# Kernel optimization log

Hardware: AMD Instinct MI355X
Metric: run time of the kernel (lower is better)

## Reference

```python
import jax, jax.numpy as jnp
import numpy as np

H = 64
N_G, E_G = 30000, 60000
N_LG, E_LG = 60000, 60000


def setup_inputs() -> dict:
    key = jax.random.key(0)
    ks = jax.random.split(key, 30)
    rn = lambda k, s, sc=0.05: jax.random.normal(k, s, jnp.float32) * sc
    return {
        "gx": jax.random.normal(ks[0], (N_G, 20), jnp.float32),
        "g_edge_index": jax.random.randint(ks[1], (2, E_G), 0, N_G, jnp.int32),
        "g_edge_attr": jax.random.uniform(ks[2], (E_G, 4), dtype=jnp.float32),
        "lgx": jax.random.normal(ks[3], (N_LG, 5), jnp.float32),
        "lg_edge_index": jax.random.randint(ks[4], (2, E_LG), 0, N_LG, jnp.int32),
        "lg_edge_attr": jax.random.uniform(ks[5], (E_LG, 1), dtype=jnp.float32),
        "adduct": jax.random.normal(ks[6], (3,), jnp.float32),
        "lin0_w": rn(ks[7], (20, H)), "lin0_b": rn(ks[8], (H,)),
        "g_nn_w1": rn(ks[9], (4, H)), "g_nn_b1": rn(ks[10], (H,)),
        "g_nn_w2": rn(ks[11], (H, H * H), 0.01), "g_nn_b2": rn(ks[12], (H * H,), 0.01),
        "g_root": rn(ks[13], (H, H)), "g_bias": rn(ks[14], (H,)),
        "lin0_lg_w": rn(ks[15], (5, H)), "lin0_lg_b": rn(ks[16], (H,)),
        "lg_nn_w1": rn(ks[17], (1, H)), "lg_nn_b1": rn(ks[18], (H,)),
        "lg_nn_w2": rn(ks[19], (H, H * H), 0.01), "lg_nn_b2": rn(ks[20], (H * H,), 0.01),
        "lg_root": rn(ks[21], (H, H)), "lg_bias": rn(ks[22], (H,)),
        "bott_w": rn(ks[23], (H + H + 3, 384)), "bott_b": rn(ks[24], (384,)),
        "lin1_w": rn(ks[25], (384, 384)), "lin1_b": rn(ks[26], (384,)),
        "lin2_w": rn(ks[27], (384, 1)), "lin2_b": rn(ks[28], (1,)),
    }


def _ecc_branch(x_in, edge_index, edge_attr, w1, b1, w2, b2, root, bias, n_iters, num_nodes):
    """N iterations of NNConv(aggr='mean') + ReLU, then sum pool over nodes."""
    src, tgt = edge_index[0], edge_index[1]  # source->target flow (PyG default)
    # edge MLP -> per-edge [in, out] weight (edge_attr is loop-invariant, compute once)
    W = (jax.nn.relu(edge_attr @ w1 + b1) @ w2 + b2).reshape(-1, H, H)  # [E, H, H]
    cnt = jnp.maximum(
        jax.ops.segment_sum(jnp.ones((tgt.shape[0],), x_in.dtype), tgt, num_segments=num_nodes),
        1.0,
    )
    x = x_in
    for _ in range(n_iters):
        msg = jnp.einsum('ei,eio->eo', x[src], W)  # gather + batched matvec
        agg = jax.ops.segment_sum(msg, tgt, num_segments=num_nodes) / cnt[:, None]  # scatter-mean
        x = jax.nn.relu(x @ root + agg + bias)  # root transform + bias (NNConv defaults)
    return x.sum(axis=0)  # sum pooling -> [H]


def reference(gx, g_edge_index, g_edge_attr, lgx, lg_edge_index, lg_edge_attr, adduct,
              lin0_w, lin0_b, g_nn_w1, g_nn_b1, g_nn_w2, g_nn_b2, g_root, g_bias,
              lin0_lg_w, lin0_lg_b, lg_nn_w1, lg_nn_b1, lg_nn_w2, lg_nn_b2, lg_root, lg_bias,
              bott_w, bott_b, lin1_w, lin1_b, lin2_w, lin2_b):
    out_g = _ecc_branch(jax.nn.relu(gx @ lin0_w + lin0_b), g_edge_index, g_edge_attr,
                        g_nn_w1, g_nn_b1, g_nn_w2, g_nn_b2, g_root, g_bias, 3, N_G)
    out_lg = _ecc_branch(jax.nn.relu(lgx @ lin0_lg_w + lin0_lg_b), lg_edge_index, lg_edge_attr,
                         lg_nn_w1, lg_nn_b1, lg_nn_w2, lg_nn_b2, lg_root, lg_bias, 3, N_LG)
    out = jnp.concatenate([out_g, out_lg, adduct], axis=-1)  # [131]
    out = jax.nn.relu(out @ bott_w + bott_b)
    for _ in range(6):
        out = jax.nn.relu(out @ lin1_w + lin1_b)
    return out @ lin2_w + lin2_b  # [1]
```

## Files before the change

kernel.cpp:

```cpp
#include <hip/hip_runtime.h>

typedef unsigned short u16;
using short8_t  = __attribute__((ext_vector_type(8)))  short;
using float16_t = __attribute__((ext_vector_type(16))) float;
using float2v   = __attribute__((ext_vector_type(2)))  float;

#define NKT 260
#define DEG_CAP 32

__device__ __forceinline__ float bf2f(u16 b) { return __uint_as_float(((unsigned)b) << 16); }
__device__ __forceinline__ u16 f2bf(float f) {
  unsigned u = __float_as_uint(f);
  return (u16)((u + 0x7fffu + ((u >> 16) & 1u)) >> 16);
}

union U8 { short8_t s; uint4 v; unsigned u[4]; };

__device__ __forceinline__ short8_t scale8r(U8 xr, float2v h2) {
  U8 out;
  #pragma unroll
  for (int p = 0; p < 4; ++p) {
    float2v r;
    r[0] = __uint_as_float(xr.u[p] << 16);
    r[1] = __uint_as_float(xr.u[p] & 0xffff0000u);
    r = r * h2;
    out.u[p] = __builtin_amdgcn_perm(__float_as_uint(r[1]), __float_as_uint(r[0]), 0x07060302);
  }
  return out.s;
}

template<int IN>
__device__ __forceinline__ void affine_body(
    const float* __restrict__ Xin, const float* __restrict__ W, const float* __restrict__ Bv,
    u16* __restrict__ Xout, int N, int gid)
{
  int n = gid >> 6, o = gid & 63;
  if (n >= N) return;
  float acc = Bv[o];
  #pragma unroll
  for (int i = 0; i < IN; ++i)
    acc = fmaf(Xin[n * IN + i], W[i * 64 + o], acc);
  Xout[gid] = f2bf(fmaxf(acc, 0.f));
}

__global__ __launch_bounds__(256) void affine_all_kernel(
    const float* __restrict__ gx, const float* __restrict__ l0w, const float* __restrict__ l0b, u16* __restrict__ xg,
    const float* __restrict__ lgx, const float* __restrict__ llw, const float* __restrict__ llb, u16* __restrict__ xl,
    const float* __restrict__ gea, const float* __restrict__ gw1, const float* __restrict__ gb1, u16* __restrict__ hg,
    const float* __restrict__ lea, const float* __restrict__ lw1, const float* __restrict__ lb1, u16* __restrict__ hl,
    int B0, int B1, int B2, int NG, int NLG, int EG, int ELG)
{
  int b = blockIdx.x, t = threadIdx.x;
  if (b < B0)       affine_body<20>(gx, l0w, l0b, xg, NG, b * 256 + t);
  else if (b < B1)  affine_body<5>(lgx, llw, llb, xl, NLG, (b - B0) * 256 + t);
  else if (b < B2)  affine_body<4>(gea, gw1, gb1, hg, EG, (b - B1) * 256 + t);
  else              affine_body<1>(lea, lw1, lb1, hl, ELG, (b - B2) * 256 + t);
}

__device__ __forceinline__ void bpack_body(
    const float* __restrict__ w2, const float* __restrict__ b2, u16* __restrict__ Bp, int gid)
{
  if (gid >= NKT * 128) return;
  int lane = gid & 63;
  int nt = (gid >> 6) & 1;
  int kt = gid >> 7;
  int o = nt * 32 + (lane & 31);
  int kbase = kt * 16 + (lane >> 5) * 8;
  u16 vals[8];
  #pragma unroll
  for (int j = 0; j < 8; ++j) {
    int k = kbase + j;
    vals[j] = f2bf((k < 4096) ? w2[(k >> 6) * 4096 + (k & 63) * 64 + o]
                              : b2[(k - 4096) * 64 + o]);
  }
  uint4 pack;
  pack.x = (unsigned)vals[0] | ((unsigned)vals[1] << 16);
  pack.y = (unsigned)vals[2] | ((unsigned)vals[3] << 16);
  pack.z = (unsigned)vals[4] | ((unsigned)vals[5] << 16);
  pack.w = (unsigned)vals[6] | ((unsigned)vals[7] << 16);
  *(uint4*)(Bp + (size_t)gid * 8) = pack;
}

__device__ __forceinline__ void rootpack_body(const float* __restrict__ root, u16* __restrict__ Rp, int gid)
{
  if (gid >= 512) return;
  int lane = gid & 63;
  int nt = (gid >> 6) & 1;
  int kt = gid >> 7;
  int o = nt * 32 + (lane & 31);
  int kbase = kt * 16 + (lane >> 5) * 8;
  u16 vals[8];
  #pragma unroll
  for (int j = 0; j < 8; ++j) vals[j] = f2bf(root[(kbase + j) * 64 + o]);
  uint4 pack;
  pack.x = (unsigned)vals[0] | ((unsigned)vals[1] << 16);
  pack.y = (unsigned)vals[2] | ((unsigned)vals[3] << 16);
  pack.z = (unsigned)vals[4] | ((unsigned)vals[5] << 16);
  pack.w = (unsigned)vals[6] | ((unsigned)vals[7] << 16);
  *(uint4*)(Rp + (size_t)gid * 8) = pack;
}

__global__ __launch_bounds__(256) void pack_all_kernel(
    const float* __restrict__ gw2, const float* __restrict__ gb2, u16* __restrict__ bpg,
    const float* __restrict__ lw2, const float* __restrict__ lb2, u16* __restrict__ bpl,
    const float* __restrict__ groot, u16* __restrict__ rpg,
    const float* __restrict__ lroot, u16* __restrict__ rpl)
{
  int b = blockIdx.x, t = threadIdx.x;
  if (b < 130)       bpack_body(gw2, gb2, bpg, b * 256 + t);
  else if (b < 260)  bpack_body(lw2, lb2, bpl, (b - 130) * 256 + t);
  else if (b < 262)  rootpack_body(groot, rpg, (b - 260) * 256 + t);
  else               rootpack_body(lroot, rpl, (b - 262) * 256 + t);
}

__device__ __forceinline__ void hist_body(
    const int* __restrict__ eidx, int* __restrict__ cnt, int* __restrict__ elist, int E, int e)
{
  if (e < E) {
    int tg = eidx[E + e];
    int pos = atomicAdd(cnt + tg, 1);
    if (pos < DEG_CAP) elist[(size_t)tg * DEG_CAP + pos] = e;
  }
}

__global__ __launch_bounds__(256) void hist_kernel(
    const int* __restrict__ eig, int* __restrict__ cg, int* __restrict__ elg, int Eg, int nbg,
    const int* __restrict__ eil, int* __restrict__ cl, int* __restrict__ ell, int El)
{
  int b = blockIdx.x, t = threadIdx.x;
  if (b < nbg) hist_body(eig, cg, elg, Eg, b * 256 + t);
  else         hist_body(eil, cl, ell, El, (b - nbg) * 256 + t);
}

__global__ __launch_bounds__(256, 2) void msg_gemm_kernel(
    const u16* __restrict__ Xg, const u16* __restrict__ Hg, const u16* __restrict__ Bg,
    const int* __restrict__ eig, u16* __restrict__ Mg, int Eg, int nbg,
    const u16* __restrict__ Xl, const u16* __restrict__ Hl, const u16* __restrict__ Bl,
    const int* __restrict__ eil, u16* __restrict__ Ml, int El)
{
  __shared__ __align__(16) u16 sB[4][8192];

  const int b = blockIdx.x;
  const u16 *X, *Hh, *Bp; const int* eidx; u16* msg; int E, e0;
  if (b < nbg) { X = Xg; Hh = Hg; Bp = Bg; eidx = eig; msg = Mg; E = Eg; e0 = b * 256; }
  else         { X = Xl; Hh = Hl; Bp = Bl; eidx = eil; msg = Ml; E = El; e0 = (b - nbg) * 256; }

  const int t = threadIdx.x;
  const int lane = t & 63;
  const int wid = t >> 6;
  const int ml = lane & 31;
  const int q  = lane >> 5;

  #pragma unroll
  for (int c0 = 0; c0 < 3; ++c0) {
    const u16* src = Bp + (size_t)c0 * 8192 + (size_t)wid * 2048 + (size_t)lane * 8;
    u16* dst = &sB[c0][wid * 2048];
    #pragma unroll
    for (int d = 0; d < 4; ++d)
      __builtin_amdgcn_global_load_lds((const __attribute__((address_space(1))) void*)(src + d * 512),
                                       (__attribute__((address_space(3))) void*)(dst + d * 512), 16, 0, 0);
  }

  const int ea  = e0 + wid * 64 + ml;
  const int eb  = ea + 32;
  const int eac = ea < E ? ea : E - 1;
  const int ebc = eb < E ? eb : E - 1;
  const int sa  = eidx[eac], sb = eidx[ebc];

  U8 xra[4], xrb[4];
  {
    const u16* xpa = X + (size_t)sa * 64 + q * 8;
    const u16* xpb = X + (size_t)sb * 64 + q * 8;
    #pragma unroll
    for (int s = 0; s < 4; ++s) {
      xra[s].v = *(const uint4*)(xpa + s * 16);
      xrb[s].v = *(const uint4*)(xpb + s * 16);
    }
  }

  const uint4* ha4 = (const uint4*)(Hh + (size_t)eac * 64);
  const uint4* hb4 = (const uint4*)(Hh + (size_t)ebc * 64);
  uint4 hc0 = ha4[0], hn0 = ha4[1];
  uint4 hc1 = hb4[0], hn1 = hb4[1];

  float16_t acc00, acc01, acc10, acc11;
  #pragma unroll
  for (int i = 0; i < 16; ++i) { acc00[i] = 0.f; acc01[i] = 0.f; acc10[i] = 0.f; acc11[i] = 0.f; }

  const u16* bsrc = Bp + (size_t)3 * 8192 + (size_t)wid * 2048 + (size_t)lane * 8;

  const short8_t* sb8 = (const short8_t*)&sB[0][0];

  asm volatile("s_waitcnt vmcnt(0)" ::: "memory");
  __builtin_amdgcn_sched_barrier(0);
  __builtin_amdgcn_s_barrier();

  for (int g = 0; g < 8; ++g) {
    #pragma unroll
    for (int cc = 0; cc < 4; ++cc) {
      {
        #pragma unroll
        for (int d = 0; d < 4; ++d)
          __builtin_amdgcn_global_load_lds((const __attribute__((address_space(1))) void*)(bsrc + d * 512),
                                           (__attribute__((address_space(3))) void*)(&sB[(cc + 3) & 3][wid * 2048] + d * 512), 16, 0, 0);
        bsrc += 8192;
      }
      unsigned w0 = ((const unsigned*)&hc0)[cc];
      unsigned w1 = ((const unsigned*)&hc1)[cc];
      const int sbase = (cc & 3) * 1024;
      #pragma unroll
      for (int hh = 0; hh < 2; ++hh) {
        float2v h20, h21;
        h20[0] = h20[1] = bf2f((u16)(hh ? (w0 >> 16) : (w0 & 0xffffu)));
        h21[0] = h21[1] = bf2f((u16)(hh ? (w1 >> 16) : (w1 & 0xffffu)));
        #pragma unroll
        for (int tt = 0; tt < 4; ++tt) {
          short8_t b0 = sb8[sbase + (hh * 4 + tt) * 128 + lane];
          short8_t b1 = sb8[sbase + (hh * 4 + tt) * 128 + 64 + lane];
          short8_t a0 = scale8r(xra[tt], h20);
          short8_t a1 = scale8r(xrb[tt], h21);
          acc00 = __builtin_amdgcn_mfma_f32_32x32x16_bf16(a0, b0, acc00, 0, 0, 0);
          acc01 = __builtin_amdgcn_mfma_f32_32x32x16_bf16(a0, b1, acc01, 0, 0, 0);
          acc10 = __builtin_amdgcn_mfma_f32_32x32x16_bf16(a1, b0, acc10, 0, 0, 0);
          acc11 = __builtin_amdgcn_mfma_f32_32x32x16_bf16(a1, b1, acc11, 0, 0, 0);
        }
      }
      asm volatile("s_waitcnt lgkmcnt(0)" ::: "memory");
      asm volatile("s_waitcnt vmcnt(8)" ::: "memory");
      __builtin_amdgcn_sched_barrier(0);
      __builtin_amdgcn_s_barrier();
    }
    hc0 = hn0; hc1 = hn1;
    if (g < 6) { hn0 = ha4[g + 2]; hn1 = hb4[g + 2]; }
  }

  {
    float2v h2; h2[0] = 1.0f; h2[1] = 1.0f;
    #pragma unroll
    for (int tt = 0; tt < 4; ++tt) {
      short8_t b0 = sb8[tt * 128 + lane];
      short8_t b1 = sb8[tt * 128 + 64 + lane];
      short8_t a0 = scale8r(xra[tt], h2);
      short8_t a1 = scale8r(xrb[tt], h2);
      acc00 = __builtin_amdgcn_mfma_f32_32x32x16_bf16(a0, b0, acc00, 0, 0, 0);
      acc01 = __builtin_amdgcn_mfma_f32_32x32x16_bf16(a0, b1, acc01, 0, 0, 0);
      acc10 = __builtin_amdgcn_mfma_f32_32x32x16_bf16(a1, b0, acc10, 0, 0, 0);
      acc11 = __builtin_amdgcn_mfma_f32_32x32x16_bf16(a1, b1, acc11, 0, 0, 0);
    }
  }

  #pragma unroll
  for (int reg = 0; reg < 16; ++reg) {
    int row = (reg & 3) + 8 * (reg >> 2) + 4 * q;
    int e1 = e0 + wid * 64 + row;
    int e2 = e1 + 32;
    if (e1 < E) {
      msg[(size_t)e1 * 64 + ml]      = f2bf(acc00[reg]);
      msg[(size_t)e1 * 64 + 32 + ml] = f2bf(acc01[reg]);
    }
    if (e2 < E) {
      msg[(size_t)e2 * 64 + ml]      = f2bf(acc10[reg]);
      msg[(size_t)e2 * 64 + 32 + ml] = f2bf(acc11[reg]);
    }
  }
}

__global__ __launch_bounds__(256, 4) void update_kernel(
    const u16* __restrict__ Xig, const u16* __restrict__ Mgg, const int* __restrict__ cg,
    const int* __restrict__ elg, const u16* __restrict__ rpg, const float* __restrict__ bg,
    u16* __restrict__ Xog, int Ng, int nbg,
    const u16* __restrict__ Xil, const u16* __restrict__ Mgl, const int* __restrict__ cl,
    const int* __restrict__ ell, const u16* __restrict__ rpl, const float* __restrict__ bl,
    u16* __restrict__ Xol, int Nl)
{
  const int b = blockIdx.x;
  const u16 *Xin, *rootp, *msg; const float *bias; const int *cnt, *elist;
  u16* Xout; int N, n0;
  if (b < nbg) { Xin=Xig; msg=Mgg; cnt=cg; elist=elg; rootp=rpg; bias=bg; Xout=Xog; N=Ng; n0=b*128; }
  else         { Xin=Xil; msg=Mgl; cnt=cl; elist=ell; rootp=rpl; bias=bl; Xout=Xol; N=Nl; n0=(b-nbg)*128; }

  const int t = threadIdx.x;
  const int lane = t & 63;
  const int wid = t >> 6;
  const int ml = lane & 31;
  const int q  = lane >> 5;
  const int nbase = n0 + wid * 32;

  const int na = nbase + ml;
  const int nac = na < N ? na : N - 1;

  U8 xr[4];
  {
    const u16* xp = Xin + (size_t)nac * 64 + q * 8;
    #pragma unroll
    for (int s = 0; s < 4; ++s) xr[s].v = *(const uint4*)(xp + s * 16);
  }
  U8 rp[8];
  {
    const uint4* rpv = (const uint4*)rootp;
    #pragma unroll
    for (int i = 0; i < 8; ++i) rp[i].v = rpv[i * 64 + lane];
  }
  const float bias0 = bias[ml], bias1 = bias[32 + ml];

  float16_t acc0, acc1;
  #pragma unroll
  for (int i = 0; i < 16; ++i) { acc0[i] = 0.f; acc1[i] = 0.f; }
  #pragma unroll
  for (int kt = 0; kt < 4; ++kt) {
    acc0 = __builtin_amdgcn_mfma_f32_32x32x16_bf16(xr[kt].s, rp[kt * 2 + 0].s, acc0, 0, 0, 0);
    acc1 = __builtin_amdgcn_mfma_f32_32x32x16_bf16(xr[kt].s, rp[kt * 2 + 1].s, acc1, 0, 0, 0);
  }

  #pragma unroll
  for (int reg = 0; reg < 16; ++reg) {
    int row = (reg & 3) + 8 * (reg >> 2) + 4 * q;
    int nn = nbase + row;
    if (nn < N) {
      int c = cnt[nn];
      int cc = c < DEG_CAP ? c : DEG_CAP;
      const int* ep = elist + (size_t)nn * DEG_CAP;
      float a0 = 0.f, a1 = 0.f;
      int j = 0;
      for (; j + 4 <= cc; j += 4) {
        int e0i = ep[j], e1i = ep[j + 1], e2i = ep[j + 2], e3i = ep[j + 3];
        u16 m00 = msg[(size_t)e0i * 64 + ml], m01 = msg[(size_t)e0i * 64 + 32 + ml];
        u16 m10 = msg[(size_t)e1i * 64 + ml], m11 = msg[(size_t)e1i * 64 + 32 + ml];
        u16 m20 = msg[(size_t)e2i * 64 + ml], m21 = msg[(size_t)e2i * 64 + 32 + ml];
        u16 m30 = msg[(size_t)e3i * 64 + ml], m31 = msg[(size_t)e3i * 64 + 32 + ml];
        a0 += bf2f(m00) + bf2f(m10) + bf2f(m20) + bf2f(m30);
        a1 += bf2f(m01) + bf2f(m11) + bf2f(m21) + bf2f(m31);
      }
      for (; j < cc; ++j) {
        int e = ep[j];
        a0 += bf2f(msg[(size_t)e * 64 + ml]);
        a1 += bf2f(msg[(size_t)e * 64 + 32 + ml]);
      }
      float rc = (c > 1) ? (1.0f / (float)c) : 1.0f;
      float o0 = fmaxf(acc0[reg] + a0 * rc + bias0, 0.f);
      float o1 = fmaxf(acc1[reg] + a1 * rc + bias1, 0.f);
      Xout[(size_t)nn * 64 + ml]      = f2bf(o0);
      Xout[(size_t)nn * 64 + 32 + ml] = f2bf(o1);
    }
  }
}

__device__ __forceinline__ void pool_body(const u16* __restrict__ X, float* __restrict__ out64,
                                          int nchunks, int bid, int t)
{
  __shared__ float red[64];
  if (t < 64) red[t] = 0.f;
  __syncthreads();
  int gid = bid * 256 + t;
  float s[8];
  #pragma unroll
  for (int j = 0; j < 8; ++j) s[j] = 0.f;
  for (int i = gid; i < nchunks; i += 256 * 256) {
    uint4 v = ((const uint4*)X)[i];
    s[0] += bf2f((u16)(v.x & 0xffffu)); s[1] += bf2f((u16)(v.x >> 16));
    s[2] += bf2f((u16)(v.y & 0xffffu)); s[3] += bf2f((u16)(v.y >> 16));
    s[4] += bf2f((u16)(v.z & 0xffffu)); s[5] += bf2f((u16)(v.z >> 16));
    s[6] += bf2f((u16)(v.w & 0xffffu)); s[7] += bf2f((u16)(v.w >> 16));
  }
  int cg = (gid & 7) * 8;
  #pragma unroll
  for (int j = 0; j < 8; ++j) atomicAdd(red + cg + j, s[j]);
  __syncthreads();
  if (t < 64) atomicAdd(out64 + t, red[t]);
}

__global__ __launch_bounds__(256) void pool_kernel(
    const u16* __restrict__ Xg, float* __restrict__ og, int ncg,
    const u16* __restrict__ Xl, float* __restrict__ ol, int ncl)
{
  int b = blockIdx.x, t = threadIdx.x;
  if (b < 256) pool_body(Xg, og, ncg, b, t);
  else         pool_body(Xl, ol, ncl, b - 256, t);
}

__global__ __launch_bounds__(256) void prep_head_kernel(
    const float* __restrict__ pg, const float* __restrict__ plg, const float* __restrict__ adduct,
    float* __restrict__ v)
{
  int t = threadIdx.x;
  if (t < 131) v[t] = (t < 64) ? pg[t] : (t < 128 ? plg[t - 64] : adduct[t - 128]);
}

__global__ __launch_bounds__(256) void gemv_relu_kernel(
    const float* __restrict__ in, const float* __restrict__ W, const float* __restrict__ b,
    float* __restrict__ out, int Ni, int No)
{
  __shared__ float red[16][17];
  int t = threadIdx.x;
  int ol = t & 15, ig = t >> 4;
  int o = blockIdx.x * 16 + ol;
  float s = 0.f;
  for (int i = ig; i < Ni; i += 16)
    s = fmaf(in[i], W[i * No + o], s);
  red[ig][ol] = s;
  __syncthreads();
  if (t < 16) {
    int oo = blockIdx.x * 16 + t;
    float acc = b[oo];
    #pragma unroll
    for (int g = 0; g < 16; ++g) acc += red[g][t];
    out[oo] = fmaxf(acc, 0.f);
  }
}

__global__ __launch_bounds__(384) void final_kernel(
    const float* __restrict__ u, const float* __restrict__ l2w, const float* __restrict__ l2b,
    float* __restrict__ out)
{
  __shared__ float wred[6];
  int t = threadIdx.x;
  float p = u[t] * l2w[t];
  #pragma unroll
  for (int off = 32; off > 0; off >>= 1) p += __shfl_down(p, off);
  if ((t & 63) == 0) wred[t >> 6] = p;
  __syncthreads();
  if (t == 0) {
    float s = l2b[0];
    #pragma unroll
    for (int i = 0; i < 6; ++i) s += wred[i];
    out[0] = s;
  }
}

extern "C" void kernel_launch(void* const* d_in, const int* in_sizes, int n_in,
                              void* d_out, int out_size, void* d_ws, size_t ws_size,
                              hipStream_t stream)
{
  const int NG = 30000, EG = 60000, NLG = 60000, ELG = 60000;

  const float* gx      = (const float*)d_in[0];
  const int*   g_ei    = (const int*)  d_in[1];
  const float* g_ea    = (const float*)d_in[2];
  const float* lgx     = (const float*)d_in[3];
  const int*   lg_ei   = (const int*)  d_in[4];
  const float* lg_ea   = (const float*)d_in[5];
  const float* adduct  = (const float*)d_in[6];
  const float* lin0_w  = (const float*)d_in[7];
  const float* lin0_b  = (const float*)d_in[8];
  const float* g_w1    = (const float*)d_in[9];
  const float* g_b1    = (const float*)d_in[10];
  const float* g_w2    = (const float*)d_in[11];
  const float* g_b2    = (const float*)d_in[12];
  const float* g_root  = (const float*)d_in[13];
  const float* g_bias  = (const float*)d_in[14];
  const float* l0lg_w  = (const float*)d_in[15];
  const float* l0lg_b  = (const float*)d_in[16];
  const float* lg_w1   = (const float*)d_in[17];
  const float* lg_b1   = (const float*)d_in[18];
  const float* lg_w2   = (const float*)d_in[19];
  const float* lg_b2   = (const float*)d_in[20];
  const float* lg_root = (const float*)d_in[21];
  const float* lg_bias = (const float*)d_in[22];
  const float* bott_w  = (const float*)d_in[23];
  const float* bott_b  = (const float*)d_in[24];
  const float* lin1_w  = (const float*)d_in[25];
  const float* lin1_b  = (const float*)d_in[26];
  const float* lin2_w  = (const float*)d_in[27];
  const float* lin2_b  = (const float*)d_in[28];

  char* p = (char*)d_ws;
  auto alloc = [&](size_t bytes) { char* r = p; p += (bytes + 255) & ~(size_t)255; return r; };
  u16*   xg_a   = (u16*)  alloc((size_t)NG  * 64 * 2);
  u16*   xg_b   = (u16*)  alloc((size_t)NG  * 64 * 2);
  u16*   xl_a   = (u16*)  alloc((size_t)NLG * 64 * 2);
  u16*   xl_b   = (u16*)  alloc((size_t)NLG * 64 * 2);
  u16*   h_g    = (u16*)  alloc((size_t)EG  * 64 * 2);
  u16*   h_l    = (u16*)  alloc((size_t)ELG * 64 * 2);
  u16*   bp_g   = (u16*)  alloc((size_t)NKT * 128 * 8 * 2 + 49152);
  u16*   bp_l   = (u16*)  alloc((size_t)NKT * 128 * 8 * 2 + 49152);
  u16*   rp_g   = (u16*)  alloc(512 * 8 * 2);
  u16*   rp_l   = (u16*)  alloc(512 * 8 * 2);
  u16*   msg_g  = (u16*)  alloc((size_t)EG  * 64 * 2);
  u16*   msg_l  = (u16*)  alloc((size_t)ELG * 64 * 2);
  int*   cnt_g  = (int*)  alloc((size_t)NG  * 4);
  int*   cnt_l  = (int*)  alloc((size_t)NLG * 4);
  int*   el_g   = (int*)  alloc((size_t)NG  * DEG_CAP * 4);
  int*   el_l   = (int*)  alloc((size_t)NLG * DEG_CAP * 4);
  float* pool_g = (float*)alloc(64 * 4);
  float* pool_l = (float*)alloc(64 * 4);
  float* hv     = (float*)alloc(131 * 4);
  float* h0     = (float*)alloc(384 * 4);
  float* h1     = (float*)alloc(384 * 4);

  const int B0 = NG * 64 / 256, B1 = B0 + NLG * 64 / 256, B2 = B1 + EG * 64 / 256;
  const int Btot = B2 + ELG * 64 / 256;
  affine_all_kernel<<<Btot, 256, 0, stream>>>(
      gx, lin0_w, lin0_b, xg_a, lgx, l0lg_w, l0lg_b, xl_a,
      g_ea, g_w1, g_b1, h_g, lg_ea, lg_w1, lg_b1, h_l,
      B0, B1, B2, NG, NLG, EG, ELG);
  pack_all_kernel<<<264, 256, 0, stream>>>(g_w2, g_b2, bp_g, lg_w2, lg_b2, bp_l,
                                           g_root, rp_g, lg_root, rp_l);
  hipMemsetAsync(cnt_g, 0, (size_t)((char*)cnt_l - (char*)cnt_g) + (size_t)NLG * 4, stream);
  const int nhg = (EG + 255) / 256, nhl = (ELG + 255) / 256;
  hist_kernel<<<nhg + nhl, 256, 0, stream>>>(g_ei, cnt_g, el_g, EG, nhg, lg_ei, cnt_l, el_l, ELG);

  const int nbg_m = (EG + 255) / 256, nbl_m = (ELG + 255) / 256;
  const int nbg_u = (NG + 127) / 128, nbl_u = (NLG + 127) / 128;
  u16 *xgc = xg_a, *xgn = xg_b, *xlc = xl_a, *xln = xl_b;
  for (int it = 0; it < 3; ++it) {
    msg_gemm_kernel<<<nbg_m + nbl_m, 256, 0, stream>>>(
        xgc, h_g, bp_g, g_ei, msg_g, EG, nbg_m,
        xlc, h_l, bp_l, lg_ei, msg_l, ELG);
    update_kernel<<<nbg_u + nbl_u, 256, 0, stream>>>(
        xgc, msg_g, cnt_g, el_g, rp_g, g_bias, xgn, NG, nbg_u,
        xlc, msg_l, cnt_l, el_l, rp_l, lg_bias, xln, NLG);
    u16* tmp = xgc; xgc = xgn; xgn = tmp;
    tmp = xlc; xlc = xln; xln = tmp;
  }

  hipMemsetAsync(pool_g, 0, (size_t)((char*)pool_l - (char*)pool_g) + 64 * 4, stream);
  pool_kernel<<<512, 256, 0, stream>>>(xgc, pool_g, NG * 8, xlc, pool_l, NLG * 8);

  prep_head_kernel<<<1, 256, 0, stream>>>(pool_g, pool_l, adduct, hv);
  gemv_relu_kernel<<<24, 256, 0, stream>>>(hv, bott_w, bott_b, h0, 131, 384);
  float* ua = h0; float* ub = h1;
  for (int L = 0; L < 6; ++L) {
    gemv_relu_kernel<<<24, 256, 0, stream>>>(ua, lin1_w, lin1_b, ub, 384, 384);
    float* tmp = ua; ua = ub; ub = tmp;
  }
  final_kernel<<<1, 384, 0, stream>>>(ua, lin2_w, lin2_b, (float*)d_out);
}
```

Baseline: 491.8 us.

## Fuse MLP head into single block kernel and fold memsets into kernels

Replaces the prep, seven gemv launches and final kernel with one 384-thread head kernel that reduces the per-block pool partials, then runs the bottleneck, six hidden layers and output layer, keeping activations in shared memory. Pool blocks now write partial sums instead of using global atomics, so the pool memset goes away. The count-buffer memset is folded into the affine kernel as extra zeroing blocks. This removes roughly ten launches and their gaps, but the head GEMVs now run on a single block that reads about 590KB of weights serially per layer.

```diff
diff --git a/kernel.cpp b/kernel.cpp
--- a/kernel.cpp
+++ b/kernel.cpp
@@ -48,13 +48,18 @@
     const float* __restrict__ lgx, const float* __restrict__ llw, const float* __restrict__ llb, u16* __restrict__ xl,
     const float* __restrict__ gea, const float* __restrict__ gw1, const float* __restrict__ gb1, u16* __restrict__ hg,
     const float* __restrict__ lea, const float* __restrict__ lw1, const float* __restrict__ lb1, u16* __restrict__ hl,
-    int B0, int B1, int B2, int NG, int NLG, int EG, int ELG)
+    int B0, int B1, int B2, int B3, int NG, int NLG, int EG, int ELG,
+    int* __restrict__ zero_ptr, int NZ)
 {
   int b = blockIdx.x, t = threadIdx.x;
   if (b < B0)       affine_body<20>(gx, l0w, l0b, xg, NG, b * 256 + t);
   else if (b < B1)  affine_body<5>(lgx, llw, llb, xl, NLG, (b - B0) * 256 + t);
   else if (b < B2)  affine_body<4>(gea, gw1, gb1, hg, EG, (b - B1) * 256 + t);
-  else              affine_body<1>(lea, lw1, lb1, hl, ELG, (b - B2) * 256 + t);
+  else if (b < B3)  affine_body<1>(lea, lw1, lb1, hl, ELG, (b - B2) * 256 + t);
+  else {
+    int idx = (b - B3) * 256 + t;
+    if (idx < NZ) zero_ptr[idx] = 0;
+  }
 }
 
 __device__ __forceinline__ void bpack_body(
@@ -345,7 +350,7 @@
   }
 }
 
-__device__ __forceinline__ void pool_body(const u16* __restrict__ X, float* __restrict__ out64,
+__device__ __forceinline__ void pool_body(const u16* __restrict__ X, float* __restrict__ part,
                                           int nchunks, int bid, int t)
 {
   __shared__ float red[64];
@@ -366,64 +371,81 @@
   #pragma unroll
   for (int j = 0; j < 8; ++j) atomicAdd(red + cg + j, s[j]);
   __syncthreads();
-  if (t < 64) atomicAdd(out64 + t, red[t]);
+  if (t < 64) part[bid * 64 + t] = red[t];
 }
 
 __global__ __launch_bounds__(256) void pool_kernel(
-    const u16* __restrict__ Xg, float* __restrict__ og, int ncg,
-    const u16* __restrict__ Xl, float* __restrict__ ol, int ncl)
+    const u16* __restrict__ Xg, float* __restrict__ pg_part, int ncg,
+    const u16* __restrict__ Xl, float* __restrict__ pl_part, int ncl)
 {
   int b = blockIdx.x, t = threadIdx.x;
-  if (b < 256) pool_body(Xg, og, ncg, b, t);
-  else         pool_body(Xl, ol, ncl, b - 256, t);
-}
-
-__global__ __launch_bounds__(256) void prep_head_kernel(
-    const float* __restrict__ pg, const float* __restrict__ plg, const float* __restrict__ adduct,
-    float* __restrict__ v)
-{
-  int t = threadIdx.x;
-  if (t < 131) v[t] = (t < 64) ? pg[t] : (t < 128 ? plg[t - 64] : adduct[t - 128]);
-}
-
-__global__ __launch_bounds__(256) void gemv_relu_kernel(
-    const float* __restrict__ in, const float* __restrict__ W, const float* __restrict__ b,
-    float* __restrict__ out, int Ni, int No)
-{
-  __shared__ float red[16][17];
-  int t = threadIdx.x;
-  int ol = t & 15, ig = t >> 4;
-  int o = blockIdx.x * 16 + ol;
-  float s = 0.f;
-  for (int i = ig; i < Ni; i += 16)
-    s = fmaf(in[i], W[i * No + o], s);
-  red[ig][ol] = s;
+  if (b < 256) pool_body(Xg, pg_part, ncg, b, t);
+  else         pool_body(Xl, pl_part, ncl, b - 256, t);
+}
+
+__global__ __launch_bounds__(384) void head_kernel(
+    const float* __restrict__ ppg, const float* __restrict__ ppl, const float* __restrict__ adduct,
+    const float* __restrict__ bw, const float* __restrict__ bb,
+    const float* __restrict__ l1w, const float* __restrict__ l1b,
+    const float* __restrict__ l2w, const float* __restrict__ l2b,
+    float* __restrict__ out)
+{
+  __shared__ float hv[131];
+  __shared__ float u[384];
+  __shared__ float wred[6];
+  const int t = threadIdx.x;
+
+  if (t < 64) {
+    float s = 0.f;
+    for (int b = 0; b < 256; ++b) s += ppg[b * 64 + t];
+    hv[t] = s;
+  } else if (t < 128) {
+    float s = 0.f;
+    for (int b = 0; b < 256; ++b) s += ppl[b * 64 + (t - 64)];
+    hv[t] = s;
+  } else if (t < 131) {
+    hv[t] = adduct[t - 128];
+  }
   __syncthreads();
-  if (t < 16) {
-    int oo = blockIdx.x * 16 + t;
-    float acc = b[oo];
-    #pragma unroll
-    for (int g = 0; g < 16; ++g) acc += red[g][t];
-    out[oo] = fmaxf(acc, 0.f);
-  }
-}
-
-__global__ __launch_bounds__(384) void final_kernel(
-    const float* __restrict__ u, const float* __restrict__ l2w, const float* __restrict__ l2b,
-    float* __restrict__ out)
-{
-  __shared__ float wred[6];
-  int t = threadIdx.x;
-  float p = u[t] * l2w[t];
-  #pragma unroll
-  for (int off = 32; off > 0; off >>= 1) p += __shfl_down(p, off);
-  if ((t & 63) == 0) wred[t >> 6] = p;
+
+  {
+    float acc = bb[t];
+    #pragma unroll 1
+    for (int g = 0; g < 16; ++g) {
+      float s = 0.f;
+      for (int i = g; i < 131; i += 16) s = fmaf(hv[i], bw[i * 384 + t], s);
+      acc += s;
+    }
+    u[t] = fmaxf(acc, 0.f);
+  }
   __syncthreads();
-  if (t == 0) {
-    float s = l2b[0];
-    #pragma unroll
-    for (int i = 0; i < 6; ++i) s += wred[i];
-    out[0] = s;
+
+  for (int L = 0; L < 6; ++L) {
+    float acc = l1b[t];
+    #pragma unroll 1
+    for (int g = 0; g < 16; ++g) {
+      float s = 0.f;
+      #pragma unroll 4
+      for (int i = g; i < 384; i += 16) s = fmaf(u[i], l1w[i * 384 + t], s);
+      acc += s;
+    }
+    __syncthreads();
+    u[t] = fmaxf(acc, 0.f);
+    __syncthreads();
+  }
+
+  {
+    float p = u[t] * l2w[t];
+    #pragma unroll
+    for (int off = 32; off > 0; off >>= 1) p += __shfl_down(p, off);
+    if ((t & 63) == 0) wred[t >> 6] = p;
+    __syncthreads();
+    if (t == 0) {
+      float s = l2b[0];
+      #pragma unroll
+      for (int i = 0; i < 6; ++i) s += wred[i];
+      out[0] = s;
+    }
   }
 }
 
@@ -481,21 +503,19 @@
   int*   cnt_l  = (int*)  alloc((size_t)NLG * 4);
   int*   el_g   = (int*)  alloc((size_t)NG  * DEG_CAP * 4);
   int*   el_l   = (int*)  alloc((size_t)NLG * DEG_CAP * 4);
-  float* pool_g = (float*)alloc(64 * 4);
-  float* pool_l = (float*)alloc(64 * 4);
-  float* hv     = (float*)alloc(131 * 4);
-  float* h0     = (float*)alloc(384 * 4);
-  float* h1     = (float*)alloc(384 * 4);
+  float* pp_g   = (float*)alloc(256 * 64 * 4);
+  float* pp_l   = (float*)alloc(256 * 64 * 4);
 
   const int B0 = NG * 64 / 256, B1 = B0 + NLG * 64 / 256, B2 = B1 + EG * 64 / 256;
-  const int Btot = B2 + ELG * 64 / 256;
-  affine_all_kernel<<<Btot, 256, 0, stream>>>(
+  const int B3 = B2 + ELG * 64 / 256;
+  const int NZ = (int)(((size_t)((char*)cnt_l - (char*)cnt_g)) / 4) + NLG;
+  const int zb = (NZ + 255) / 256;
+  affine_all_kernel<<<B3 + zb, 256, 0, stream>>>(
       gx, lin0_w, lin0_b, xg_a, lgx, l0lg_w, l0lg_b, xl_a,
       g_ea, g_w1, g_b1, h_g, lg_ea, lg_w1, lg_b1, h_l,
-      B0, B1, B2, NG, NLG, EG, ELG);
+      B0, B1, B2, B3, NG, NLG, EG, ELG, cnt_g, NZ);
   pack_all_kernel<<<264, 256, 0, stream>>>(g_w2, g_b2, bp_g, lg_w2, lg_b2, bp_l,
                                            g_root, rp_g, lg_root, rp_l);
-  hipMemsetAsync(cnt_g, 0, (size_t)((char*)cnt_l - (char*)cnt_g) + (size_t)NLG * 4, stream);
   const int nhg = (EG + 255) / 256, nhl = (ELG + 255) / 256;
   hist_kernel<<<nhg + nhl, 256, 0, stream>>>(g_ei, cnt_g, el_g, EG, nhg, lg_ei, cnt_l, el_l, ELG);
 
@@ -513,15 +533,9 @@
     tmp = xlc; xlc = xln; xln = tmp;
   }
 
-  hipMemsetAsync(pool_g, 0, (size_t)((char*)pool_l - (char*)pool_g) + 64 * 4, stream);
-  pool_kernel<<<512, 256, 0, stream>>>(xgc, pool_g, NG * 8, xlc, pool_l, NLG * 8);
-
-  prep_head_kernel<<<1, 256, 0, stream>>>(pool_g, pool_l, adduct, hv);
-  gemv_relu_kernel<<<24, 256, 0, stream>>>(hv, bott_w, bott_b, h0, 131, 384);
-  float* ua = h0; float* ub = h1;
-  for (int L = 0; L < 6; ++L) {
-    gemv_relu_kernel<<<24, 256, 0, stream>>>(ua, lin1_w, lin1_b, ub, 384, 384);
-    float* tmp = ua; ua = ub; ub = tmp;
-  }
-  final_kernel<<<1, 384, 0, stream>>>(ua, lin2_w, lin2_b, (float*)d_out);
-}
+  pool_kernel<<<512, 256, 0, stream>>>(xgc, pp_g, NG * 8, xlc, pp_l, NLG * 8);
+
+  head_kernel<<<1, 384, 0, stream>>>(pp_g, pp_l, adduct,
+                                     bott_w, bott_b, lin1_w, lin1_b, lin2_w, lin2_b,
+                                     (float*)d_out);
+}
```

Result: slower. 542.6 us (+10.3%).
